# Kernel tuning notes

Hardware: AMD Instinct MI355X
Metric: run time of the kernel (lower is better)

The kernel has to match this reference:

```python
import jax, jax.numpy as jnp
import numpy as np

NEG_SLOPE = 0.2
EPS = 1e-16

N_NODES = 50000
N_EDGES = 1600000
IN_CH = 256
HID = 16
HEADS = 2


def setup_inputs() -> dict:
    key = jax.random.key(0)
    ks = jax.random.split(key, 12)
    s = lambda k, shape, scale=0.1: jax.random.normal(k, shape, dtype=jnp.float32) * scale
    x = jax.random.normal(ks[0], (N_NODES, IN_CH), dtype=jnp.float32)
    edge_index = jax.random.randint(ks[1], (2, N_EDGES), 0, N_NODES, dtype=jnp.int64)
    return {
        "x": x,
        "edge_index": edge_index,
        "W1": s(ks[2], (IN_CH, HEADS * HID)),
        "att_src1": s(ks[3], (HEADS, HID)),
        "att_dst1": s(ks[4], (HEADS, HID)),
        "b1": jnp.zeros((HEADS * HID,), jnp.float32),
        "W2": s(ks[5], (HEADS * HID, HID)),
        "att_src2": s(ks[6], (1, HID)),
        "att_dst2": s(ks[7], (1, HID)),
        "b2": jnp.zeros((HID,), jnp.float32),
        "Wm1": s(ks[8], (2 * HID, HID)),
        "bm1": jnp.zeros((HID,), jnp.float32),
        "Wm2": s(ks[9], (HID, 1)),
        "bm2": jnp.zeros((1,), jnp.float32),
    }


def gat_conv(x, src, dst, W, att_src, att_dst, bias, heads, out_ch, concat):
    # x: [N, F] -> h: [N, H, C]
    n = x.shape[0]
    h = (x @ W).reshape(n, heads, out_ch)
    # per-node attention logits [N, H]
    a_src = jnp.sum(h * att_src, axis=-1)
    a_dst = jnp.sum(h * att_dst, axis=-1)
    # per-edge logits: message j (src) -> i (dst); softmax grouped by dst
    e = a_src[src] + a_dst[dst]                      # [E, H]
    e = jax.nn.leaky_relu(e, NEG_SLOPE)
    e_max = jax.ops.segment_max(e, dst, num_segments=n)
    e_exp = jnp.exp(e - e_max[dst])
    denom = jax.ops.segment_sum(e_exp, dst, num_segments=n)
    alpha = e_exp / (denom[dst] + EPS)               # [E, H]
    msg = alpha[:, :, None] * h[src]                 # [E, H, C]
    out = jax.ops.segment_sum(msg, dst, num_segments=n)  # [N, H, C]
    out = out.reshape(n, heads * out_ch) if concat else out.mean(axis=1)
    return out + bias


def reference(x, edge_index, W1, att_src1, att_dst1, b1,
              W2, att_src2, att_dst2, b2, Wm1, bm1, Wm2, bm2):
    src, dst = edge_index[0], edge_index[1]
    # eval mode: feature/attention dropout are identity
    h = gat_conv(x, src, dst, W1, att_src1, att_dst1, b1, HEADS, HID, concat=True)
    h = jax.nn.elu(h)
    h = gat_conv(h, src, dst, W2, att_src2, att_dst2, b2, 1, HID, concat=False)
    # edge MLP on gathered (src, dst) node pairs
    ef = jnp.concatenate([h[src], h[dst]], axis=-1)  # [E, 2*HID]
    ef = jax.nn.relu(ef @ Wm1 + bm1)
    flow = (ef @ Wm2 + bm2).squeeze(-1)              # [E]
    return jax.nn.relu(flow)
```

## Files before the change

kernel.cpp:

```cpp
#include <hip/hip_runtime.h>
#include <hip/hip_bf16.h>
#include <hip/hip_fp16.h>

#define N_NODES 50000
#define N_EDGES 1600000
#define IN_CH 256
#define NEG_SLOPE 0.2f
#define EPS_F 1e-16f
#define CNT_PAD 16
#define CAP 128
#define NBK 196
#define CAPB 10240
#define PCHUNK 3125
#define KTILE 64
#define XS_PITCH (KTILE + 4)

__device__ __forceinline__ float lrelu(float x) {
    return x > 0.f ? x : NEG_SLOPE * x;
}

__device__ __forceinline__ float2 h2f(unsigned int w) {
    __half2 h;
    *reinterpret_cast<unsigned int*>(&h) = w;
    return __half22float2(h);
}

__device__ __forceinline__ unsigned int f2h2(float a, float b) {
    __half2 h = __floats2half2_rn(a, b);
    return *reinterpret_cast<unsigned int*>(&h);
}

__device__ __forceinline__ int detect_i64(const int* __restrict__ ei) {
    const int lane = threadIdx.x & 63;
    const unsigned long long b = __ballot(ei[2 * lane + 1] != 0);
    return b == 0ull ? 1 : 0;
}

__device__ __forceinline__ int ld_src(const int* ei, int f, int e) {
    return f ? ei[2 * (size_t)e] : ei[e];
}
__device__ __forceinline__ int ld_dst(const int* ei, int f, int e) {
    return f ? ei[2 * (size_t)N_EDGES + 2 * (size_t)e]
             : ei[(size_t)N_EDGES + e];
}

__global__ __launch_bounds__(1024) void k_part(const int* __restrict__ ei,
                                               int* __restrict__ gcnt,
                                               int2* __restrict__ bseg)
{
    __shared__ int hist[NBK];
    __shared__ int cur[NBK];
    const int t = threadIdx.x;
    const int f = detect_i64(ei);
    for (int j = t; j < NBK; j += 1024) hist[j] = 0;
    __syncthreads();
    const int e0 = blockIdx.x * PCHUNK;
    const int e1 = min(e0 + PCHUNK, N_EDGES);
    int es[4], ed[4];
    int ne = 0;
    #pragma unroll
    for (int q = 0; q < 4; ++q) {
        const int e = e0 + t + 1024 * q;
        if (e < e1) {
            es[ne] = ld_src(ei, f, e);
            ed[ne] = ld_dst(ei, f, e);
            ++ne;
        }
    }
    for (int q = 0; q < ne; ++q) atomicAdd(&hist[ed[q] >> 8], 1);
    __syncthreads();
    for (int j = t; j < NBK; j += 1024)
        cur[j] = j * CAPB + atomicAdd(&gcnt[j], hist[j]);
    __syncthreads();
    for (int q = 0; q < ne; ++q) {
        const int bk = ed[q] >> 8;
        const int pos = atomicAdd(&cur[bk], 1);
        if (pos - bk * CAPB < CAPB) bseg[pos] = make_int2(es[q], ed[q]);
    }
}

__global__ __launch_bounds__(1024) void k_sub(const int* __restrict__ gcnt,
                                              const int2* __restrict__ bseg,
                                              int* __restrict__ cnt,
                                              int* __restrict__ csr_src)
{
    __shared__ int cur[256];
    const int b = blockIdx.x;
    const int t = threadIdx.x;
    if (t < 256) cur[t] = 0;
    __syncthreads();
    const int count = min(gcnt[b], CAPB);
    const int2* seg = bseg + (size_t)b * CAPB;
    for (int i = t; i < count; i += 1024) {
        const int2 e = seg[i];
        const int slot = atomicAdd(&cur[e.y & 255], 1);
        if (slot < CAP) csr_src[((size_t)e.y << 7) + slot] = e.x;
    }
    __syncthreads();
    if (t < 256) {
        const int n = b * 256 + t;
        if (n < N_NODES) cnt[(size_t)n * CNT_PAD] = min(cur[t], CAP);
    }
}

__global__ __launch_bounds__(256) void k1_gemm1(
    const float* __restrict__ x, const float* __restrict__ W1,
    const float* __restrict__ att_src1, const float* __restrict__ att_dst1,
    __half* __restrict__ h1, float* __restrict__ a_src1, float* __restrict__ a_dst1)
{
    __shared__ float w1s[IN_CH * 32];
    __shared__ float xs[64 * XS_PITCH];
    __shared__ float attss[32], attds[32];
    const int t = threadIdx.x;
    for (int i = t; i < IN_CH * 32; i += 256) w1s[i] = W1[i];
    if (t < 32) { attss[t] = att_src1[t]; attds[t] = att_dst1[t]; }
    const int row0 = blockIdx.x * 64;
    const int colq = t & 7, c4 = colq * 4;
    const int rp = t >> 3;
    const int r0 = rp * 2, r1 = r0 + 1;
    float4 a0 = make_float4(0.f, 0.f, 0.f, 0.f);
    float4 a1 = make_float4(0.f, 0.f, 0.f, 0.f);
    for (int kb = 0; kb < IN_CH; kb += KTILE) {
        __syncthreads();
        #pragma unroll
        for (int i = 0; i < 4; ++i) {
            const int idx = t + 256 * i;
            const int r = idx >> 4, p = idx & 15;
            const int row = row0 + r;
            float4 vv = make_float4(0.f, 0.f, 0.f, 0.f);
            if (row < N_NODES)
                vv = *(const float4*)(x + (size_t)row * IN_CH + kb + p * 4);
            *(float4*)(&xs[r * XS_PITCH + p * 4]) = vv;
        }
        __syncthreads();
        #pragma unroll 8
        for (int kt = 0; kt < KTILE; ++kt) {
            const float xv0 = xs[r0 * XS_PITCH + kt];
            const float xv1 = xs[r1 * XS_PITCH + kt];
            const float4 wv = *(const float4*)(&w1s[(kb + kt) * 32 + c4]);
            a0.x += xv0 * wv.x; a0.y += xv0 * wv.y;
            a0.z += xv0 * wv.z; a0.w += xv0 * wv.w;
            a1.x += xv1 * wv.x; a1.y += xv1 * wv.y;
            a1.z += xv1 * wv.z; a1.w += xv1 * wv.w;
        }
    }
    const int row_a = row0 + r0, row_b = row0 + r1;
    if (row_a < N_NODES) {
        uint2 p; p.x = f2h2(a0.x, a0.y); p.y = f2h2(a0.z, a0.w);
        *(uint2*)(h1 + (size_t)row_a * 32 + c4) = p;
    }
    if (row_b < N_NODES) {
        uint2 p; p.x = f2h2(a1.x, a1.y); p.y = f2h2(a1.z, a1.w);
        *(uint2*)(h1 + (size_t)row_b * 32 + c4) = p;
    }
    float sa0 = a0.x * attss[c4] + a0.y * attss[c4 + 1]
              + a0.z * attss[c4 + 2] + a0.w * attss[c4 + 3];
    float sd0 = a0.x * attds[c4] + a0.y * attds[c4 + 1]
              + a0.z * attds[c4 + 2] + a0.w * attds[c4 + 3];
    float sa1 = a1.x * attss[c4] + a1.y * attss[c4 + 1]
              + a1.z * attss[c4 + 2] + a1.w * attss[c4 + 3];
    float sd1 = a1.x * attds[c4] + a1.y * attds[c4 + 1]
              + a1.z * attds[c4 + 2] + a1.w * attds[c4 + 3];
    sa0 += __shfl_xor(sa0, 1); sa0 += __shfl_xor(sa0, 2);
    sd0 += __shfl_xor(sd0, 1); sd0 += __shfl_xor(sd0, 2);
    sa1 += __shfl_xor(sa1, 1); sa1 += __shfl_xor(sa1, 2);
    sd1 += __shfl_xor(sd1, 1); sd1 += __shfl_xor(sd1, 2);
    const int head = colq >> 2;
    if ((colq & 3) == 0) {
        if (row_a < N_NODES) {
            a_src1[row_a * 2 + head] = sa0;
            a_dst1[row_a * 2 + head] = sd0;
        }
        if (row_b < N_NODES) {
            a_src1[row_b * 2 + head] = sa1;
            a_dst1[row_b * 2 + head] = sd1;
        }
    }
}

__global__ __launch_bounds__(256) void k_agg1f(
    const int* __restrict__ cnt, const int* __restrict__ csr_src,
    const float* __restrict__ a_src1, const float* __restrict__ a_dst1,
    const __half* __restrict__ h1,
    const float* __restrict__ b1, const float* __restrict__ W2,
    const float* __restrict__ att_src2, const float* __restrict__ att_dst2,
    __half* __restrict__ h2, float* __restrict__ a_src2, float* __restrict__ a_dst2)
{
    __shared__ float w2s[32 * 16];
    __shared__ float b1s[32], as2[16], ad2[16];
    __shared__ float act_s[16][33];
    const int t = threadIdx.x;
    for (int i = t; i < 512; i += 256) w2s[i] = W2[i];
    if (t < 32) b1s[t] = b1[t];
    if (t < 16) { as2[t] = att_src2[t]; ad2[t] = att_dst2[t]; }

    const int lane = t & 63;
    const int wv = t >> 6;
    const int g = lane >> 4;
    const int chp = lane & 15;
    const int head = chp >> 3;
    const int node = blockIdx.x * 16 + wv * 4 + g;
    const int active = (node < N_NODES);
    const int len = active ? min(cnt[(size_t)node * CNT_PAD], CAP) : 0;
    const int beg = node << 7;
    const float adh = active ? a_dst1[2 * (size_t)node + head] : 0.f;
    const unsigned int* __restrict__ h1u = (const unsigned int*)h1;
    float accx = 0.f, accy = 0.f, sw = 0.f;
    for (int bi = 0; __any(bi < len); bi += 8) {
        int s[8]; float a[8]; unsigned int hw[8]; float w[8];
        #pragma unroll
        for (int j = 0; j < 8; ++j) {
            int sv = csr_src[beg + bi + j];
            s[j] = (bi + j < len) ? sv : 0;
        }
        #pragma unroll
        for (int j = 0; j < 8; ++j) a[j] = a_src1[2 * (size_t)s[j] + head];
        #pragma unroll
        for (int j = 0; j < 8; ++j) hw[j] = h1u[(size_t)s[j] * 16 + chp];
        #pragma unroll
        for (int j = 0; j < 8; ++j)
            w[j] = (bi + j < len) ? __expf(lrelu(a[j] + adh)) : 0.f;
        #pragma unroll
        for (int j = 0; j < 8; ++j) {
            const float2 hf = h2f(hw[j]);
            sw += w[j];
            accx += w[j] * hf.x; accy += w[j] * hf.y;
        }
    }
    const float inv = 1.f / (sw + EPS_F);
    const int nl = wv * 4 + g;
    {
        float ax = accx * inv + b1s[2 * chp];
        float ay = accy * inv + b1s[2 * chp + 1];
        ax = ax > 0.f ? ax : expm1f(ax);
        ay = ay > 0.f ? ay : expm1f(ay);
        act_s[nl][2 * chp] = ax;
        act_s[nl][2 * chp + 1] = ay;
    }
    __syncthreads();
    const int nn = t >> 4;
    const int j2 = t & 15;
    const int node2 = blockIdx.x * 16 + nn;
    float acc2 = 0.f;
    #pragma unroll
    for (int k = 0; k < 32; ++k) acc2 += act_s[nn][k] * w2s[k * 16 + j2];
    if (node2 < N_NODES) h2[(size_t)node2 * 16 + j2] = __float2half(acc2);
    float sa = acc2 * as2[j2], sd = acc2 * ad2[j2];
    sa += __shfl_xor(sa, 1); sa += __shfl_xor(sa, 2);
    sa += __shfl_xor(sa, 4); sa += __shfl_xor(sa, 8);
    sd += __shfl_xor(sd, 1); sd += __shfl_xor(sd, 2);
    sd += __shfl_xor(sd, 4); sd += __shfl_xor(sd, 8);
    if (j2 == 0 && node2 < N_NODES) { a_src2[node2] = sa; a_dst2[node2] = sd; }
}

__global__ __launch_bounds__(256) void k_agg2f(
    const int* __restrict__ cnt, const int* __restrict__ csr_src,
    const float* __restrict__ a_src2, const float* __restrict__ a_dst2,
    const __half* __restrict__ h2,
    const float* __restrict__ b2, const float* __restrict__ Wm1,
    const float* __restrict__ bm1,
    __half* __restrict__ u, __half* __restrict__ v)
{
    __shared__ float wa[16 * 16], wb[16 * 16];
    __shared__ float b2s[16], bm1s[16];
    __shared__ float act_s[4][16];
    const int t = threadIdx.x;
    if (t < 256) { wa[t] = Wm1[t]; wb[t] = Wm1[256 + t]; }
    if (t < 16) { b2s[t] = b2[t]; bm1s[t] = bm1[t]; }

    const int wid = (blockIdx.x * 256 + t) >> 6;
    const int lane = t & 63;
    const int wv = t >> 6;
    const int active = (wid < N_NODES);
    const int len = active ? min(cnt[(size_t)wid * CNT_PAD], CAP) : 0;
    const int beg = wid << 7, end = beg + len;
    const float ad = active ? a_dst2[wid] : 0.f;
    const int slot = lane >> 3, chp = lane & 7;
    const int rep = (chp == 0);
    const unsigned int* __restrict__ h2u = (const unsigned int*)h2;
    float accx = 0.f, accy = 0.f, sw = 0.f;
    int i = beg + slot;
    for (; i + 24 < end; i += 32) {
        int s[4]; float a[4]; unsigned int hw[4]; float w[4];
        #pragma unroll
        for (int j = 0; j < 4; ++j) s[j] = csr_src[i + 8 * j];
        #pragma unroll
        for (int j = 0; j < 4; ++j) a[j] = a_src2[s[j]];
        #pragma unroll
        for (int j = 0; j < 4; ++j) hw[j] = h2u[(size_t)s[j] * 8 + chp];
        #pragma unroll
        for (int j = 0; j < 4; ++j) w[j] = __expf(lrelu(a[j] + ad));
        float wsum = 0.f;
        #pragma unroll
        for (int j = 0; j < 4; ++j) {
            const float2 hf = h2f(hw[j]);
            wsum += w[j];
            accx += w[j] * hf.x; accy += w[j] * hf.y;
        }
        if (rep) sw += wsum;
    }
    for (; i < end; i += 8) {
        const int s = csr_src[i];
        const float w = __expf(lrelu(a_src2[s] + ad));
        if (rep) sw += w;
        const float2 hf = h2f(h2u[(size_t)s * 8 + chp]);
        accx += w * hf.x; accy += w * hf.y;
    }
    sw += __shfl_xor(sw, 8); sw += __shfl_xor(sw, 16); sw += __shfl_xor(sw, 32);
    const float swt = __shfl(sw, 0);
    accx += __shfl_xor(accx, 8); accx += __shfl_xor(accx, 16); accx += __shfl_xor(accx, 32);
    accy += __shfl_xor(accy, 8); accy += __shfl_xor(accy, 16); accy += __shfl_xor(accy, 32);
    const float inv = 1.f / (swt + EPS_F);
    if (lane < 8) {
        float2 o;
        o.x = accx * inv + b2s[2 * chp];
        o.y = accy * inv + b2s[2 * chp + 1];
        *(float2*)(&act_s[wv][2 * chp]) = o;
    }
    __syncthreads();
    const int c = lane & 15;
    float su = bm1s[c], sv = 0.f;
    #pragma unroll
    for (int k = 0; k < 16; ++k) {
        const float a = act_s[wv][k];
        su += a * wa[k * 16 + c];
        sv += a * wb[k * 16 + c];
    }
    if (lane < 16 && active) {
        u[(size_t)wid * 16 + c] = __float2half(su);
        v[(size_t)wid * 16 + c] = __float2half(sv);
    }
}

__global__ __launch_bounds__(256) void k7_lite(
    const int* __restrict__ ei,
    const __half* __restrict__ u, const __half* __restrict__ v,
    const float* __restrict__ Wm2, const float* __restrict__ bm2,
    float* __restrict__ out)
{
    __shared__ float wm2s[16];
    __shared__ float bm2s;
    const int t = threadIdx.x;
    const int f = detect_i64(ei);
    if (t < 16) wm2s[t] = Wm2[t];
    if (t == 0) bm2s = bm2[0];
    __syncthreads();
    const int e = blockIdx.x * 256 + t;
    if (e >= N_EDGES) return;
    const int s = ld_src(ei, f, e);
    const int d = ld_dst(ei, f, e);
    const uint4* up = (const uint4*)(u + (size_t)s * 16);
    const uint4* vp = (const uint4*)(v + (size_t)d * 16);
    const uint4 ua = up[0], ub = up[1];
    const uint4 va = vp[0], vb = vp[1];
    float fl = bm2s;
    unsigned int uw[8] = {ua.x, ua.y, ua.z, ua.w, ub.x, ub.y, ub.z, ub.w};
    unsigned int vw[8] = {va.x, va.y, va.z, va.w, vb.x, vb.y, vb.z, vb.w};
    #pragma unroll
    for (int i = 0; i < 8; ++i) {
        const float2 a = h2f(uw[i]);
        const float2 b = h2f(vw[i]);
        fl += fmaxf(a.x + b.x, 0.f) * wm2s[2 * i];
        fl += fmaxf(a.y + b.y, 0.f) * wm2s[2 * i + 1];
    }
    out[e] = fmaxf(fl, 0.f);
}

extern "C" void kernel_launch(void* const* d_in, const int* in_sizes, int n_in,
                              void* d_out, int out_size, void* d_ws, size_t ws_size,
                              hipStream_t stream)
{
    const float* x        = (const float*)d_in[0];
    const int*   ei       = (const int*)d_in[1];
    const float* W1       = (const float*)d_in[2];
    const float* att_src1 = (const float*)d_in[3];
    const float* att_dst1 = (const float*)d_in[4];
    const float* b1       = (const float*)d_in[5];
    const float* W2       = (const float*)d_in[6];
    const float* att_src2 = (const float*)d_in[7];
    const float* att_dst2 = (const float*)d_in[8];
    const float* b2       = (const float*)d_in[9];
    const float* Wm1      = (const float*)d_in[10];
    const float* bm1      = (const float*)d_in[11];
    const float* Wm2      = (const float*)d_in[12];
    const float* bm2      = (const float*)d_in[13];

    float* ws = (float*)d_ws;
    size_t off = 0;
    __half* h1 = (__half*)(ws + off); off += 16 * (size_t)N_NODES;
    float* a_src1 = ws + off; off += 2  * (size_t)N_NODES;
    float* a_dst1 = ws + off; off += 2  * (size_t)N_NODES;
    __half* h2 = (__half*)(ws + off); off += 8 * (size_t)N_NODES;
    float* a_src2 = ws + off; off += 1  * (size_t)N_NODES;
    float* a_dst2 = ws + off; off += 1  * (size_t)N_NODES;
    __half* u = (__half*)(ws + off); off += 8 * (size_t)N_NODES;
    __half* v = (__half*)(ws + off); off += 8 * (size_t)N_NODES;
    int* cnt     = (int*)(ws + off);  off += (size_t)N_NODES * CNT_PAD;
    int* csr_src = (int*)(ws + off);  off += (size_t)N_NODES * CAP;
    int2* bseg   = (int2*)(ws + off); off += (size_t)NBK * CAPB * 2;
    int* gcnt    = (int*)(ws + off);  off += 256;

    hipMemsetAsync(gcnt, 0, 256 * sizeof(int), stream);
    k_part<<<(N_EDGES + PCHUNK - 1) / PCHUNK, 1024, 0, stream>>>(ei, gcnt, bseg);
    k_sub<<<NBK, 1024, 0, stream>>>(gcnt, bseg, cnt, csr_src);

    k1_gemm1<<<(N_NODES + 63) / 64, 256, 0, stream>>>(
        x, W1, att_src1, att_dst1, h1, a_src1, a_dst1);
    k_agg1f<<<(N_NODES + 15) / 16, 256, 0, stream>>>(
        cnt, csr_src, a_src1, a_dst1, h1, b1, W2, att_src2, att_dst2,
        h2, a_src2, a_dst2);
    k_agg2f<<<(N_NODES + 3) / 4, 256, 0, stream>>>(
        cnt, csr_src, a_src2, a_dst2, h2, b2, Wm1, bm1, u, v);
    k7_lite<<<(N_EDGES + 255) / 256, 256, 0, stream>>>(
        ei, u, v, Wm2, bm2, (float*)d_out);
}
```

Baseline: 251.6 us.

## Map eight nodes per wavefront in layer-2 aggregation instead of one

The layer-2 aggregation kernel now gives each 8-lane group its own destination node, so one wavefront handles 8 nodes and a block handles 32. Each group walks its node's edges serially in unrolled batches of 8, with masked loads and weights. This removes the cross-slot shuffle reductions and raises work per wave for nodes of about 32 edges. In exchange, lanes within a wave diverge by degree, since the loop runs until the longest list in the wave is done, and the same csr_src address is loaded redundantly by all 8 lanes of a group. The Wm1 projection now computes two channels per lane and writes packed half2 values.

After: 246.5 us. 2.0% less time.

```diff
diff --git a/kernel.cpp b/kernel.cpp
--- a/kernel.cpp
+++ b/kernel.cpp
@@ -263,72 +263,66 @@
 {
     __shared__ float wa[16 * 16], wb[16 * 16];
     __shared__ float b2s[16], bm1s[16];
-    __shared__ float act_s[4][16];
-    const int t = threadIdx.x;
-    if (t < 256) { wa[t] = Wm1[t]; wb[t] = Wm1[256 + t]; }
+    __shared__ float act_s[32][18];
+    const int t = threadIdx.x;
+    wa[t] = Wm1[t]; wb[t] = Wm1[256 + t];
     if (t < 16) { b2s[t] = b2[t]; bm1s[t] = bm1[t]; }
-
-    const int wid = (blockIdx.x * 256 + t) >> 6;
+    __syncthreads();
+
     const int lane = t & 63;
     const int wv = t >> 6;
-    const int active = (wid < N_NODES);
-    const int len = active ? min(cnt[(size_t)wid * CNT_PAD], CAP) : 0;
-    const int beg = wid << 7, end = beg + len;
-    const float ad = active ? a_dst2[wid] : 0.f;
-    const int slot = lane >> 3, chp = lane & 7;
-    const int rep = (chp == 0);
+    const int g = lane >> 3;
+    const int chp = lane & 7;
+    const int node = blockIdx.x * 32 + wv * 8 + g;
+    const int active = (node < N_NODES);
+    const int len = active ? min(cnt[(size_t)node * CNT_PAD], CAP) : 0;
+    const int beg = node << 7;
+    const float ad = active ? a_dst2[node] : 0.f;
     const unsigned int* __restrict__ h2u = (const unsigned int*)h2;
     float accx = 0.f, accy = 0.f, sw = 0.f;
-    int i = beg + slot;
-    for (; i + 24 < end; i += 32) {
-        int s[4]; float a[4]; unsigned int hw[4]; float w[4];
-        #pragma unroll
-        for (int j = 0; j < 4; ++j) s[j] = csr_src[i + 8 * j];
-        #pragma unroll
-        for (int j = 0; j < 4; ++j) a[j] = a_src2[s[j]];
-        #pragma unroll
-        for (int j = 0; j < 4; ++j) hw[j] = h2u[(size_t)s[j] * 8 + chp];
-        #pragma unroll
-        for (int j = 0; j < 4; ++j) w[j] = __expf(lrelu(a[j] + ad));
-        float wsum = 0.f;
-        #pragma unroll
-        for (int j = 0; j < 4; ++j) {
+    for (int bi = 0; __any(bi < len); bi += 8) {
+        int s[8]; float a[8]; unsigned int hw[8]; float w[8];
+        #pragma unroll
+        for (int j = 0; j < 8; ++j) {
+            int sv = csr_src[beg + bi + j];
+            s[j] = (bi + j < len) ? sv : 0;
+        }
+        #pragma unroll
+        for (int j = 0; j < 8; ++j) a[j] = a_src2[s[j]];
+        #pragma unroll
+        for (int j = 0; j < 8; ++j) hw[j] = h2u[(size_t)s[j] * 8 + chp];
+        #pragma unroll
+        for (int j = 0; j < 8; ++j)
+            w[j] = (bi + j < len) ? __expf(lrelu(a[j] + ad)) : 0.f;
+        #pragma unroll
+        for (int j = 0; j < 8; ++j) {
             const float2 hf = h2f(hw[j]);
-            wsum += w[j];
+            sw += w[j];
             accx += w[j] * hf.x; accy += w[j] * hf.y;
         }
-        if (rep) sw += wsum;
-    }
-    for (; i < end; i += 8) {
-        const int s = csr_src[i];
-        const float w = __expf(lrelu(a_src2[s] + ad));
-        if (rep) sw += w;
-        const float2 hf = h2f(h2u[(size_t)s * 8 + chp]);
-        accx += w * hf.x; accy += w * hf.y;
-    }
-    sw += __shfl_xor(sw, 8); sw += __shfl_xor(sw, 16); sw += __shfl_xor(sw, 32);
-    const float swt = __shfl(sw, 0);
-    accx += __shfl_xor(accx, 8); accx += __shfl_xor(accx, 16); accx += __shfl_xor(accx, 32);
-    accy += __shfl_xor(accy, 8); accy += __shfl_xor(accy, 16); accy += __shfl_xor(accy, 32);
-    const float inv = 1.f / (swt + EPS_F);
-    if (lane < 8) {
+    }
+    const float inv = 1.f / (sw + EPS_F);
+    const int nl = wv * 8 + g;
+    {
         float2 o;
         o.x = accx * inv + b2s[2 * chp];
         o.y = accy * inv + b2s[2 * chp + 1];
-        *(float2*)(&act_s[wv][2 * chp]) = o;
-    }
-    __syncthreads();
-    const int c = lane & 15;
-    float su = bm1s[c], sv = 0.f;
+        *(float2*)(&act_s[nl][2 * chp]) = o;
+    }
+    __syncthreads();
+    const int c0 = 2 * chp, c1 = c0 + 1;
+    float su0 = bm1s[c0], su1 = bm1s[c1], sv0 = 0.f, sv1 = 0.f;
     #pragma unroll
     for (int k = 0; k < 16; ++k) {
-        const float a = act_s[wv][k];
-        su += a * wa[k * 16 + c];
-        sv += a * wb[k * 16 + c];
-    }
-    if (lane < 16 && active) {
-        u[(size_t)wid * 16 + c] = __float2half(su);
-        v[(size_t)wid * 16 + c] = __float2half(sv);
+        const float a = act_s[nl][k];
+        su0 += a * wa[k * 16 + c0];
+        su1 += a * wa[k * 16 + c1];
+        sv0 += a * wb[k * 16 + c0];
+        sv1 += a * wb[k * 16 + c1];
+    }
+    if (active) {
+        *(unsigned int*)(u + (size_t)node * 16 + c0) = f2h2(su0, su1);
+        *(unsigned int*)(v + (size_t)node * 16 + c0) = f2h2(sv0, sv1);
     }
 }
 
@@ -409,7 +403,7 @@
     k_agg1f<<<(N_NODES + 15) / 16, 256, 0, stream>>>(
         cnt, csr_src, a_src1, a_dst1, h1, b1, W2, att_src2, att_dst2,
         h2, a_src2, a_dst2);
-    k_agg2f<<<(N_NODES + 3) / 4, 256, 0, stream>>>(
+    k_agg2f<<<(N_NODES + 31) / 32, 256, 0, stream>>>(
         cnt, csr_src, a_src2, a_dst2, h2, b2, Wm1, bm1, u, v);
     k7_lite<<<(N_EDGES + 255) / 256, 256, 0, stream>>>(
         ei, u, v, Wm2, bm2, (float*)d_out);
```
